# Kernel tuning notes

Measured on AMD Instinct MI355X. Metric: run time of the kernel, lower is better.

The kernel has to match this reference:

```python
import jax, jax.numpy as jnp
import numpy as np

# 22-joint tree (parents[i] < i); feet at 18, 21; spine at 2 (stand-in for get_totalcapture_skeleton)
PARENTS = [-1, 0, 1, 2, 3, 4, 3, 6, 7, 8, 3, 10, 11, 12, 1, 14, 15, 16, 17, 1, 19, 20]
FEET = [18, 21]
SPINE = 2
LAMBDAS = dict(root=5.0, rot=1.0, pos=2.0, vel=1.0, smooth=0.5, contact=2.0, floor=2.0, tilt=1.0)


def _normalize(x, eps=1e-12):
    return x / jnp.maximum(jnp.linalg.norm(x, axis=-1, keepdims=True), eps)


def cont6d_to_mat(d6):
    # d6: (..., 6) -> (..., 3, 3) with columns (b1, b2, b3)
    a1, a2 = d6[..., :3], d6[..., 3:]
    b1 = _normalize(a1)
    b2 = _normalize(a2 - b1 * jnp.sum(b1 * a2, axis=-1, keepdims=True))
    b3 = jnp.cross(b1, b2)
    return jnp.stack((b1, b2, b3), axis=-1)


def run_canonical_fk(full_output, offsets):
    # full_output: (B, S, 22, 6); root forced to identity rot / zero pos
    B, S, J, _ = full_output.shape
    rot_mats = cont6d_to_mat(full_output)  # (B, S, 22, 3, 3)
    eye = jnp.broadcast_to(jnp.eye(3, dtype=full_output.dtype), (B, S, 3, 3))
    zeros = jnp.zeros((B, S, 3), dtype=full_output.dtype)
    g_rots = [None] * J
    g_pos = [None] * J
    g_rots[0], g_pos[0] = eye, zeros
    for i in range(1, J):
        p = PARENTS[i]
        g_rots[i] = jnp.einsum('bsij,bsjk->bsik', g_rots[p], rot_mats[:, :, i])
        g_pos[i] = g_pos[p] + jnp.einsum('bsij,j->bsi', g_rots[p], offsets[i])
    return jnp.stack(g_pos, axis=2)  # (B, S, 22, 3)


def mse(a, b):
    return jnp.mean(jnp.square(a - b))


def motion_loss(pred_full, target_full, offsets):
    l_root = mse(pred_full[:, :, 0, :3], target_full[:, :, 0, :3]) + \
             mse(pred_full[:, :, 1, :], target_full[:, :, 1, :])
    l_rot = mse(pred_full[:, :, 2:], target_full[:, :, 2:])

    pred_pos = run_canonical_fk(pred_full, offsets)
    gt_pos = run_canonical_fk(target_full, offsets)
    l_pos = mse(pred_pos, gt_pos)

    pred_vel = pred_pos[:, 1:] - pred_pos[:, :-1]
    gt_vel = gt_pos[:, 1:] - gt_pos[:, :-1]
    l_vel = mse(pred_vel, gt_vel)

    pred_acc = pred_vel[:, 1:] - pred_vel[:, :-1]
    gt_acc = gt_vel[:, 1:] - gt_vel[:, :-1]
    l_smooth = mse(pred_acc, gt_acc)

    feet = jnp.array(FEET)
    l_floor = mse(pred_pos[:, :, feet, 1], gt_pos[:, :, feet, 1])

    gt_feet_vel = gt_vel[:, :, feet, :]
    pred_feet_vel = pred_vel[:, :, feet, :]
    is_planted = (jnp.linalg.norm(gt_feet_vel, axis=-1) < 0.005).astype(pred_full.dtype)
    l_contact = jnp.mean(jnp.linalg.norm(pred_feet_vel, axis=-1) * is_planted)

    pred_spine = cont6d_to_mat(pred_full[:, :, SPINE])
    gt_spine = cont6d_to_mat(target_full[:, :, SPINE])
    # R @ [0,1,0]^T == second column of R
    l_tilt = mse(pred_spine[..., :, 1], gt_spine[..., :, 1])

    total = (LAMBDAS['root'] * l_root + LAMBDAS['rot'] * l_rot + LAMBDAS['pos'] * l_pos +
             LAMBDAS['vel'] * l_vel + LAMBDAS['smooth'] * l_smooth + LAMBDAS['contact'] * l_contact +
             LAMBDAS['floor'] * l_floor + LAMBDAS['tilt'] * l_tilt)
    return total


def setup_inputs() -> dict:
    key = jax.random.key(0)
    k1, k2 = jax.random.split(key)
    B, S, J, C = 256, 512, 22, 6
    pred_full = jax.random.normal(k1, (B, S, J, C), dtype=jnp.float32)
    target_full = jax.random.normal(k2, (B, S, J, C), dtype=jnp.float32)
    rng = np.random.default_rng(42)
    off = rng.normal(size=(J, 3)).astype(np.float32) * 0.1
    off[0] = 0.0
    offsets = jnp.asarray(off)
    return {"pred_full": pred_full, "target_full": target_full, "offsets": offsets}


def reference(pred_full, target_full, offsets):
    return motion_loss(pred_full, target_full, offsets)
```

## Files before the change

### kernel.cpp

```cpp
#include <hip/hip_runtime.h>

namespace {

constexpr int kB = 256;
constexpr int kS = 512;
constexpr int CHUNK  = 62;
constexpr int NCHUNK = 9;
constexpr int NSLOT  = 64;
constexpr int BUFF   = 1536;
constexpr int LDSF   = 3 * BUFF;

constexpr float BSf   = 131072.f;
constexpr float K_R1  = 5.0f / (BSf * 3.f);
constexpr float K_R2  = 5.0f / (BSf * 6.f);
constexpr float K_ROT = 1.0f / (BSf * 120.f);
constexpr float K_POS = 2.0f / (BSf * 66.f);
constexpr float K_VEL = 1.0f / (256.f * 511.f * 66.f);
constexpr float K_SMO = 0.5f / (256.f * 510.f * 66.f);
constexpr float K_FLO = 2.0f / (BSf * 2.f);
constexpr float K_CON = 2.0f / (256.f * 511.f * 2.f);
constexpr float K_TIL = 1.0f / (BSf * 3.f);

__device__ __forceinline__ void cont6d(const float a[6], float R[3][3]) {
    float n1 = a[0]*a[0] + a[1]*a[1] + a[2]*a[2];
    float i1 = __frsqrt_rn(fmaxf(n1, 1e-24f));
    float b1x = a[0]*i1, b1y = a[1]*i1, b1z = a[2]*i1;
    float dp  = b1x*a[3] + b1y*a[4] + b1z*a[5];
    float ux = a[3] - b1x*dp, uy = a[4] - b1y*dp, uz = a[5] - b1z*dp;
    float n2 = ux*ux + uy*uy + uz*uz;
    float i2 = __frsqrt_rn(fmaxf(n2, 1e-24f));
    float b2x = ux*i2, b2y = uy*i2, b2z = uz*i2;
    R[0][0] = b1x; R[1][0] = b1y; R[2][0] = b1z;
    R[0][1] = b2x; R[1][1] = b2y; R[2][1] = b2z;
    R[0][2] = b1y*b2z - b1z*b2y;
    R[1][2] = b1z*b2x - b1x*b2z;
    R[2][2] = b1x*b2y - b1y*b2x;
}

template<bool NEED_R, bool SPINE_J, bool FOOT>
__device__ __forceinline__ void joint_step(
    const float aP[6], const float aT[6], const float* __restrict__ off,
    const float RpP[3][3], const float ppP[3], float RnP[3][3], float pnP[3],
    const float RpT[3][3], const float ppT[3], float RnT[3][3], float pnT[3],
    float wf, float wv, float wa, float& s)
{
    float dsum = 0.f;
    #pragma unroll
    for (int k = 0; k < 6; ++k) { float dd = aP[k] - aT[k]; dsum += dd*dd; }
    s += wf * (K_ROT * dsum);

    const float ox = off[0], oy = off[1], oz = off[2];
    #pragma unroll
    for (int r = 0; r < 3; ++r) {
        pnP[r] = ppP[r] + RpP[r][0]*ox + RpP[r][1]*oy + RpP[r][2]*oz;
        pnT[r] = ppT[r] + RpT[r][0]*ox + RpT[r][1]*oy + RpT[r][2]*oz;
    }

    if constexpr (NEED_R) {
        float RlP[3][3], RlT[3][3];
        cont6d(aP, RlP);
        cont6d(aT, RlT);
        if constexpr (SPINE_J) {
            float t0 = RlP[0][1] - RlT[0][1];
            float t1 = RlP[1][1] - RlT[1][1];
            float t2 = RlP[2][1] - RlT[2][1];
            s += wf * (K_TIL * (t0*t0 + t1*t1 + t2*t2));
        }
        #pragma unroll
        for (int r = 0; r < 3; ++r)
            #pragma unroll
            for (int c = 0; c < 3; ++c) {
                RnP[r][c] = RpP[r][0]*RlP[0][c] + RpP[r][1]*RlP[1][c] + RpP[r][2]*RlP[2][c];
                RnT[r][c] = RpT[r][0]*RlT[0][c] + RpT[r][1]*RlT[1][c] + RpT[r][2]*RlT[2][c];
            }
    }

    float d[3], d1[3];
    #pragma unroll
    for (int r = 0; r < 3; ++r) d[r] = pnP[r] - pnT[r];
    s += wf * (K_POS * (d[0]*d[0] + d[1]*d[1] + d[2]*d[2]));

    float va = 0.f, sa = 0.f;
    #pragma unroll
    for (int r = 0; r < 3; ++r) {
        d1[r]    = __shfl_down(d[r], 1);
        float d2 = __shfl_down(d[r], 2);
        float dv = d1[r] - d[r];            va += dv*dv;
        float ds = d2 - 2.f*d1[r] + d[r];   sa += ds*ds;
    }
    s += wv * (K_VEL * va);
    s += wa * (K_SMO * sa);

    if constexpr (FOOT) {
        s += wf * (K_FLO * (d[1]*d[1]));
        float gx = __shfl_down(pnT[0], 1) - pnT[0];
        float gy = __shfl_down(pnT[1], 1) - pnT[1];
        float gz = __shfl_down(pnT[2], 1) - pnT[2];
        float pvx = gx + (d1[0] - d[0]);
        float pvy = gy + (d1[1] - d[1]);
        float pvz = gz + (d1[2] - d[2]);
        float planted = (gx*gx + gy*gy + gz*gz < 2.5e-5f) ? 1.f : 0.f;
        s += wv * (K_CON * (planted * sqrtf(pvx*pvx + pvy*pvy + pvz*pvz)));
    }
}

__global__ __launch_bounds__(64)
void motion_loss_kernel(const float* __restrict__ pred,
                        const float* __restrict__ targ,
                        const float* __restrict__ offs,
                        float* __restrict__ acc)
{
    __shared__ float lds[LDSF];

    const int lane = threadIdx.x;
    const int cg    = blockIdx.x;
    const int b     = cg / NCHUNK;
    const int chunk = cg - b * NCHUNK;
    const int s0    = chunk * CHUNK;
    const int s     = s0 + lane;

    const float wf = (lane < CHUNK && s     < kS) ? 1.f : 0.f;
    const float wv = (lane < CHUNK && s + 1 < kS) ? 1.f : 0.f;
    const float wa = (lane < CHUNK && s + 2 < kS) ? 1.f : 0.f;

    const float* predb = pred + (size_t)b * kS * 132;
    const float* targb = targ + (size_t)b * kS * 132;

    auto issue = [&](int FB, float* buf) {
        #pragma unroll
        for (int r = 0; r < 6; ++r) {
            const float* tb = (r < 3) ? predb : targb;
            int uu = (r % 3) * 64 + lane;
            int f  = uu / 3;
            int c  = uu - f * 3;
            int sf = s0 + f; sf = (sf < kS) ? sf : (kS - 1);
            const float* src = tb + (size_t)sf * 132 + FB + 4 * c;
            __builtin_amdgcn_global_load_lds(
                (const __attribute__((address_space(1))) void*)src,
                (__attribute__((address_space(3))) void*)(buf + r * 256),
                16, 0, 0);
        }
    };

    float* buf0 = lds;
    float* buf1 = lds + BUFF;
    float* buf2 = lds + 2 * BUFF;

    #define VW(N) do { asm volatile("s_waitcnt vmcnt(" #N ")" ::: "memory"); \
                       __builtin_amdgcn_sched_barrier(0); } while (0)
    #define LW0   do { asm volatile("s_waitcnt lgkmcnt(0)" ::: "memory"); \
                       __builtin_amdgcn_sched_barrier(0); } while (0)

    auto rd6 = [&](const float* base, int jj, float a[6]) {
        const float2* q = reinterpret_cast<const float2*>(base + jj * 6);
        float2 x = q[0], y = q[1], z = q[2];
        a[0]=x.x; a[1]=x.y; a[2]=y.x; a[3]=y.y; a[4]=z.x; a[5]=z.y;
    };

    issue(0,  buf0);
    issue(12, buf1);
    issue(24, buf2);

    float loss = 0.f;
    float R1P[3][3], R3P[3][3], RAP[3][3], RBP[3][3];
    float R1T[3][3], R3T[3][3], RAT[3][3], RBT[3][3];
    float p1[3], p3P[3], pAP[3], pBP[3], pSP[3];
    float          p3T[3], pAT[3], pBT[3], pST[3];
    auto& p1P = p1; auto& p1T = p1;

    #define RD2(BUF) float aP0[6], aT0[6], aP1[6], aT1[6]; { \
        const float* pb_ = (BUF) + lane * 12; \
        const float* tb_ = (BUF) + 768 + lane * 12; \
        rd6(pb_, 0, aP0); rd6(tb_, 0, aT0); rd6(pb_, 1, aP1); rd6(tb_, 1, aT1); }

    #define JS(AP, AT, J, NR, SP, FT, RP, PP, RN, PN) \
        joint_step<NR, SP, FT>(AP, AT, offs + (J)*3, \
            RP##P, PP##P, RN##P, PN##P, RP##T, PP##T, RN##T, PN##T, \
            wf, wv, wa, loss)

    VW(12);
    {
        RD2(buf0);
        LW0; issue(36, buf0);
        {
            float d0 = aP0[0]-aT0[0], d1 = aP0[1]-aT0[1], d2 = aP0[2]-aT0[2];
            loss += wf * (K_R1 * (d0*d0 + d1*d1 + d2*d2));
        }
        {
            float dsum = 0.f;
            #pragma unroll
            for (int k = 0; k < 6; ++k) { float dd = aP1[k]-aT1[k]; dsum += dd*dd; }
            loss += wf * (K_R2 * dsum);
            cont6d(aP1, R1P);
            cont6d(aT1, R1T);
            p1[0] = offs[3]; p1[1] = offs[4]; p1[2] = offs[5];
        }
    }
    VW(12);
    {
        RD2(buf1);
        LW0; issue(48, buf1);
        JS(aP0, aT0,  2, true , true , false, R1, p1, RA, pA);
        JS(aP1, aT1,  3, true , false, false, RA, pA, R3, p3);
    }
    VW(12);
    {
        RD2(buf2);
        LW0; issue(60, buf2);
        JS(aP0, aT0,  4, true , false, false, R3, p3, RA, pA);
        JS(aP1, aT1,  5, false, false, false, RA, pA, RB, pS);
    }
    VW(12);
    {
        RD2(buf0);
        LW0; issue(72, buf0);
        JS(aP0, aT0,  6, true , false, false, R3, p3, RA, pA);
        JS(aP1, aT1,  7, true , false, false, RA, pA, RB, pB);
    }
    VW(12);
    {
        RD2(buf1);
        LW0; issue(84, buf1);
        JS(aP0, aT0,  8, true , false, false, RB, pB, RA, pA);
        JS(aP1, aT1,  9, false, false, false, RA, pA, RB, pS);
    }
    VW(12);
    {
        RD2(buf2);
        LW0; issue(96, buf2);
        JS(aP0, aT0, 10, true , false, false, R3, p3, RB, pB);
        JS(aP1, aT1, 11, true , false, false, RB, pB, RA, pA);
    }
    VW(12);
    {
        RD2(buf0);
        LW0; issue(108, buf0);
        JS(aP0, aT0, 12, true , false, false, RA, pA, RB, pB);
        JS(aP1, aT1, 13, false, false, false, RB, pB, RA, pS);
    }
    VW(12);
    {
        RD2(buf1);
        LW0; issue(120, buf1);
        JS(aP0, aT0, 14, true , false, false, R1, p1, RA, pA);
        JS(aP1, aT1, 15, true , false, false, RA, pA, RB, pB);
    }
    VW(12);
    {
        RD2(buf2);
        JS(aP0, aT0, 16, true , false, false, RB, pB, RA, pA);
        JS(aP1, aT1, 17, true , false, false, RA, pA, RB, pB);
    }
    VW(6);
    {
        RD2(buf0);
        JS(aP0, aT0, 18, false, false, true , RB, pB, RA, pS);
        JS(aP1, aT1, 19, true , false, false, R1, p1, RA, pA);
    }
    VW(0);
    {
        RD2(buf1);
        JS(aP0, aT0, 20, true , false, false, RA, pA, RB, pB);
        JS(aP1, aT1, 21, false, false, true , RB, pB, RA, pS);
    }
    #undef JS
    #undef RD2
    #undef VW
    #undef LW0

    float v = loss;
    #pragma unroll
    for (int o = 32; o > 0; o >>= 1) v += __shfl_xor(v, o);
    if (lane == 0) atomicAdd(&acc[cg & (NSLOT - 1)], v);
}

__global__ void finalize_kernel(const float* __restrict__ acc, float* __restrict__ out) {
    float v = acc[threadIdx.x];
    #pragma unroll
    for (int o = 32; o > 0; o >>= 1) v += __shfl_xor(v, o);
    if (threadIdx.x == 0) out[0] = v;
}

}

extern "C" void kernel_launch(void* const* d_in, const int* in_sizes, int n_in,
                              void* d_out, int out_size, void* d_ws, size_t ws_size,
                              hipStream_t stream) {
    const float* pred = (const float*)d_in[0];
    const float* targ = (const float*)d_in[1];
    const float* offs = (const float*)d_in[2];
    float* acc = (float*)d_ws;

    hipMemsetAsync(acc, 0, NSLOT * sizeof(float), stream);
    motion_loss_kernel<<<dim3(kB * NCHUNK), dim3(64), 0, stream>>>(pred, targ, offs, acc);
    finalize_kernel<<<1, 64, 0, stream>>>(acc, (float*)d_out);
}
```

Before: 62.62 us.

## Pack four waves per block and shrink LDS ring to double buffering

Each block now holds four independent 64-lane wavefronts, each with its own LDS region, instead of one wave per block. The per-wave prefetch ring drops from three buffers to two, which halves the loads kept in flight and lowers the per-wave LDS footprint. The aim is to cut block launch overhead and fit more waves per CU. The cost is a shallower prefetch, which leaves less time to hide global load latency.

Result: slower. 65.12 us (+4.0%).

```diff
diff --git a/kernel.cpp b/kernel.cpp
--- a/kernel.cpp
+++ b/kernel.cpp
@@ -7,8 +7,9 @@
 constexpr int CHUNK  = 62;
 constexpr int NCHUNK = 9;
 constexpr int NSLOT  = 64;
+constexpr int WPB    = 4;
 constexpr int BUFF   = 1536;
-constexpr int LDSF   = 3 * BUFF;
+constexpr int WLDS   = 2 * BUFF;
 
 constexpr float BSf   = 131072.f;
 constexpr float K_R1  = 5.0f / (BSf * 3.f);
@@ -104,16 +105,19 @@
     }
 }
 
-__global__ __launch_bounds__(64)
+__global__ __launch_bounds__(64 * WPB)
 void motion_loss_kernel(const float* __restrict__ pred,
                         const float* __restrict__ targ,
                         const float* __restrict__ offs,
                         float* __restrict__ acc)
 {
-    __shared__ float lds[LDSF];
-
-    const int lane = threadIdx.x;
-    const int cg    = blockIdx.x;
+    __shared__ float lds[WPB][WLDS];
+
+    const int tid  = threadIdx.x;
+    const int wid  = tid >> 6;
+    const int lane = tid & 63;
+
+    const int cg    = blockIdx.x * WPB + wid;
     const int b     = cg / NCHUNK;
     const int chunk = cg - b * NCHUNK;
     const int s0    = chunk * CHUNK;
@@ -142,9 +146,8 @@
         }
     };
 
-    float* buf0 = lds;
-    float* buf1 = lds + BUFF;
-    float* buf2 = lds + 2 * BUFF;
+    float* buf0 = lds[wid];
+    float* buf1 = lds[wid] + BUFF;
 
     #define VW(N) do { asm volatile("s_waitcnt vmcnt(" #N ")" ::: "memory"); \
                        __builtin_amdgcn_sched_barrier(0); } while (0)
@@ -159,7 +162,6 @@
 
     issue(0,  buf0);
     issue(12, buf1);
-    issue(24, buf2);
 
     float loss = 0.f;
     float R1P[3][3], R3P[3][3], RAP[3][3], RBP[3][3];
@@ -178,10 +180,10 @@
             RP##P, PP##P, RN##P, PN##P, RP##T, PP##T, RN##T, PN##T, \
             wf, wv, wa, loss)
 
-    VW(12);
-    {
-        RD2(buf0);
-        LW0; issue(36, buf0);
+    VW(6);
+    {
+        RD2(buf0);
+        LW0; issue(24, buf0);
         {
             float d0 = aP0[0]-aT0[0], d1 = aP0[1]-aT0[1], d2 = aP0[2]-aT0[2];
             loss += wf * (K_R1 * (d0*d0 + d1*d1 + d2*d2));
@@ -196,70 +198,71 @@
             p1[0] = offs[3]; p1[1] = offs[4]; p1[2] = offs[5];
         }
     }
-    VW(12);
-    {
-        RD2(buf1);
-        LW0; issue(48, buf1);
+    VW(6);
+    {
+        RD2(buf1);
+        LW0; issue(36, buf1);
         JS(aP0, aT0,  2, true , true , false, R1, p1, RA, pA);
         JS(aP1, aT1,  3, true , false, false, RA, pA, R3, p3);
     }
-    VW(12);
-    {
-        RD2(buf2);
-        LW0; issue(60, buf2);
+    VW(6);
+    {
+        RD2(buf0);
+        LW0; issue(48, buf0);
         JS(aP0, aT0,  4, true , false, false, R3, p3, RA, pA);
         JS(aP1, aT1,  5, false, false, false, RA, pA, RB, pS);
     }
-    VW(12);
-    {
-        RD2(buf0);
-        LW0; issue(72, buf0);
+    VW(6);
+    {
+        RD2(buf1);
+        LW0; issue(60, buf1);
         JS(aP0, aT0,  6, true , false, false, R3, p3, RA, pA);
         JS(aP1, aT1,  7, true , false, false, RA, pA, RB, pB);
     }
-    VW(12);
-    {
-        RD2(buf1);
-        LW0; issue(84, buf1);
+    VW(6);
+    {
+        RD2(buf0);
+        LW0; issue(72, buf0);
         JS(aP0, aT0,  8, true , false, false, RB, pB, RA, pA);
         JS(aP1, aT1,  9, false, false, false, RA, pA, RB, pS);
     }
-    VW(12);
-    {
-        RD2(buf2);
-        LW0; issue(96, buf2);
+    VW(6);
+    {
+        RD2(buf1);
+        LW0; issue(84, buf1);
         JS(aP0, aT0, 10, true , false, false, R3, p3, RB, pB);
         JS(aP1, aT1, 11, true , false, false, RB, pB, RA, pA);
     }
-    VW(12);
-    {
-        RD2(buf0);
-        LW0; issue(108, buf0);
+    VW(6);
+    {
+        RD2(buf0);
+        LW0; issue(96, buf0);
         JS(aP0, aT0, 12, true , false, false, RA, pA, RB, pB);
         JS(aP1, aT1, 13, false, false, false, RB, pB, RA, pS);
     }
-    VW(12);
-    {
-        RD2(buf1);
-        LW0; issue(120, buf1);
+    VW(6);
+    {
+        RD2(buf1);
+        LW0; issue(108, buf1);
         JS(aP0, aT0, 14, true , false, false, R1, p1, RA, pA);
         JS(aP1, aT1, 15, true , false, false, RA, pA, RB, pB);
     }
-    VW(12);
-    {
-        RD2(buf2);
+    VW(6);
+    {
+        RD2(buf0);
+        LW0; issue(120, buf0);
         JS(aP0, aT0, 16, true , false, false, RB, pB, RA, pA);
         JS(aP1, aT1, 17, true , false, false, RA, pA, RB, pB);
     }
     VW(6);
     {
-        RD2(buf0);
+        RD2(buf1);
         JS(aP0, aT0, 18, false, false, true , RB, pB, RA, pS);
         JS(aP1, aT1, 19, true , false, false, R1, p1, RA, pA);
     }
     VW(0);
     {
-        RD2(buf1);
+        RD2(buf0);
         JS(aP0, aT0, 20, true , false, false, RA, pA, RB, pB);
         JS(aP1, aT1, 21, false, false, true , RB, pB, RA, pS);
     }
@@ -292,6 +295,7 @@
     float* acc = (float*)d_ws;
 
     hipMemsetAsync(acc, 0, NSLOT * sizeof(float), stream);
-    motion_loss_kernel<<<dim3(kB * NCHUNK), dim3(64), 0, stream>>>(pred, targ, offs, acc);
+    const int nblocks = (kB * NCHUNK) / WPB;
+    motion_loss_kernel<<<dim3(nblocks), dim3(64 * WPB), 0, stream>>>(pred, targ, offs, acc);
     finalize_kernel<<<1, 64, 0, stream>>>(acc, (float*)d_out);
 }
```
